# Kernel tuning notes

Hardware: AMD Instinct MI355X
Metric: run time of the kernel (lower is better)

Reference implementation:

```python
import jax, jax.numpy as jnp
import numpy as np

B, N, K, NS = 2, 1024, 64, 32          # batch, points, keypoints (top-k), ball-query neighbors
RADIUS = 1.0                            # ball-query radius (sample_and_group)
R_VOX, S_VOX = 2.0, 0.4                 # voxelize search radius / step
NV = int(round(2 * R_VOX / S_VOX)) + 1  # 11 offsets per axis
C = NV ** 3                             # 1331 candidates per keypoint
F = 32                                  # deep feature channels (num_feat)


def _gather(data, idx):
    # data: (B, N, ...) ; idx: (B, ...) int -> (B, idx_shape..., ...)
    return jax.vmap(lambda d, i: d[i])(data, idx)


def setup_inputs() -> dict:
    key = jax.random.key(0)
    ks = jax.random.split(key, 16)
    f = lambda k, s: jax.random.normal(k, s, dtype=jnp.float32)
    return {
        "src_pts": f(ks[0], (B, 6, N)),
        "tgt_pts": f(ks[1], (B, 6, N)),
        "R_init": f(ks[2], (1, 3, 3)),
        "t_init": f(ks[3], (3, 1)),
        # feature-extraction shared MLP (6 -> 32 -> 32)
        "W1": f(ks[4], (6, F)) * 0.4, "b1": jnp.zeros((F,), jnp.float32),
        "W2": f(ks[5], (F, F)) * 0.2, "b2": jnp.zeros((F,), jnp.float32),
        # weighting (saliency) MLP (32 -> 16 -> 1)
        "Ww1": f(ks[6], (F, 16)) * 0.3, "bw1": jnp.zeros((16,), jnp.float32),
        "Ww2": f(ks[7], (16, 1)) * 0.3, "bw2": jnp.zeros((1,), jnp.float32),
        # deep-feature-embedding shared MLP (3+32 -> 32 -> 32)
        "Wd1": f(ks[8], (3 + F, F)) * 0.3, "bd1": jnp.zeros((F,), jnp.float32),
        "Wd2": f(ks[9], (F, F)) * 0.2, "bd2": jnp.zeros((F,), jnp.float32),
    }


def reference(src_pts, tgt_pts, R_init, t_init,
              W1, b1, W2, b2, Ww1, bw1, Ww2, bw2, Wd1, bd1, Wd2, bd2):
    def fe(pts):                                   # shared feature extraction (FE1)
        x = jnp.transpose(pts, (0, 2, 1))          # (B,N,6)
        h = jax.nn.relu(x @ W1 + b1)
        return x[..., :3], jax.nn.relu(h @ W2 + b2)  # xyz (B,N,3), feat (B,N,F)

    def dfe(x):                                    # shared DFE mini-PointNet MLP
        h = jax.nn.relu(x @ Wd1 + bd1)
        return jax.nn.relu(h @ Wd2 + bd2)

    src_xyz_all, src_feat = fe(src_pts)
    tgt_xyz_all, tgt_feat = fe(tgt_pts)

    # ---- weighting layer: per-point saliency, top-K keypoints ----
    score = (jax.nn.relu(src_feat @ Ww1 + bw1) @ Ww2 + bw2)[..., 0]  # (B,N)
    _, key_idx = jax.lax.top_k(score, K)                              # (B,K)

    src_pts_T = jnp.transpose(src_pts, (0, 2, 1))                     # (B,N,6)
    keypts = _gather(src_pts_T, key_idx)                              # (B,K,6)
    kxyz = keypts[..., :3]                                            # (B,K,3)

    # ---- sample_and_group: ball query among keypoints (npoint == K) ----
    sqd = jnp.sum((kxyz[:, :, None] - kxyz[:, None]) ** 2, -1)        # (B,K,K)
    gidx = jnp.broadcast_to(jnp.arange(K), (B, K, K))
    gidx = jnp.where(sqd > RADIUS ** 2, K, gidx)
    gidx = jnp.sort(gidx, -1)[:, :, :NS]
    gidx = jnp.where(gidx == K, gidx[:, :, :1], gidx)                 # (B,K,NS)

    grouped = _gather(kxyz, gidx)                                     # (B,K,NS,3)
    rel = grouped - kxyz[:, :, None]                                  # local coords
    orig_idx = _gather(key_idx, gidx)                                 # (B,K,NS) into N
    keyfeats = _gather(src_feat, orig_idx)                            # (B,K,NS,F)
    src_cat = jnp.concatenate([rel, keyfeats], -1)                    # (B,K,NS,3+F)

    # ---- voxelize: candidate grid around R_init-transformed keypoints ----
    Rm = jnp.broadcast_to(R_init, (B, 3, 3))
    kxyz_t = jnp.einsum('bij,bkj->bki', Rm, kxyz)                     # (B,K,3)
    off = jnp.linspace(-R_VOX, R_VOX, NV, dtype=jnp.float32)
    gx, gy, gz = jnp.meshgrid(off, off, off, indexing='ij')
    grid = jnp.stack([gx, gy, gz], -1).reshape(-1, 3)                 # (C,3)
    cand = kxyz_t[:, :, None, :] + grid                               # (B,K,C,3)

    # ---- 1-NN of each candidate in the target cloud (feature lookup) ----
    cn = jnp.sum(cand ** 2, -1)                                       # (B,K,C)
    tn = jnp.sum(tgt_xyz_all ** 2, -1)                                # (B,N)
    cross = jnp.einsum('bkcd,bnd->bkcn', cand, tgt_xyz_all)           # (B,K,C,N)
    d = cn[..., None] + tn[:, None, None, :] - 2.0 * cross
    nn = jnp.argmin(jax.lax.stop_gradient(d), -1)                     # (B,K,C)
    nn_xyz = _gather(tgt_xyz_all, nn)                                 # (B,K,C,3)
    nn_feat = _gather(tgt_feat, nn)                                   # (B,K,C,F)
    tgt_cat = jnp.concatenate([cand - nn_xyz, nn_feat], -1)           # (B,K,C,3+F)

    # ---- DFE embeddings + corresponding-point generation (CPG) ----
    src_emb = jnp.max(dfe(src_cat), axis=2)                           # (B,K,F)  max over neighbors
    tgt_emb = dfe(tgt_cat)                                            # (B,K,C,F)
    sim = jnp.einsum('bkd,bkcd->bkc', src_emb, tgt_emb)               # (B,K,C)
    w = jax.nn.softmax(sim, -1)
    tgt_vcp = jnp.einsum('bkc,bkcd->bkd', w, cand)                    # (B,K,3)

    return kxyz, tgt_vcp
```

## Files before the change

### kernel.cpp

```cpp
#include <hip/hip_runtime.h>
#include <math.h>

#define BB 2
#define NPTS 1024
#define KK 64
#define NSZ 32
#define CC 1331
#define FF 32
#define RAD2 1.0f
#define NCOL 121
#define NRNG 8

__global__ __launch_bounds__(64)
void k_features(const float* __restrict__ src_pts, const float* __restrict__ tgt_pts,
                const float* __restrict__ W1, const float* __restrict__ b1,
                const float* __restrict__ W2, const float* __restrict__ b2,
                const float* __restrict__ Ww1, const float* __restrict__ bw1,
                const float* __restrict__ Ww2, const float* __restrict__ bw2,
                const float* __restrict__ Wd1, const float* __restrict__ bd1,
                float* __restrict__ src_feat, float* __restrict__ tgt_A,
                float* __restrict__ tgt_m2, float* __restrict__ score)
{
    int gid = blockIdx.x * blockDim.x + threadIdx.x;
    int isTgt = gid >= BB * NPTS;
    int pn = gid & (BB * NPTS - 1);
    int b = pn >> 10, n = pn & 1023;
    const float* pts = isTgt ? tgt_pts : src_pts;
    float p[6];
#pragma unroll
    for (int i = 0; i < 6; i++) p[i] = pts[(b * 6 + i) * NPTS + n];
    float h[FF];
#pragma unroll
    for (int j = 0; j < FF; j++) {
        float a = b1[j];
#pragma unroll
        for (int i = 0; i < 6; i++) a = fmaf(p[i], W1[i * FF + j], a);
        h[j] = fmaxf(a, 0.0f);
    }
    float ft[FF];
#pragma unroll
    for (int j = 0; j < FF; j++) {
        float a = b2[j];
#pragma unroll
        for (int i = 0; i < FF; i++) a = fmaf(h[i], W2[i * FF + j], a);
        ft[j] = fmaxf(a, 0.0f);
    }
    if (isTgt) {
        float x = p[0], y = p[1], z = p[2];
        float4 v; v.x = x; v.y = y; v.z = z; v.w = x * x + y * y + z * z;
        ((float4*)tgt_m2)[b * NPTS + n] = v;
        float av[FF];
#pragma unroll
        for (int j = 0; j < FF; j++) av[j] = bd1[j];
#pragma unroll
        for (int i = 0; i < FF; i++) {
            float fi = ft[i];
#pragma unroll
            for (int j = 0; j < FF; j++)
                av[j] = fmaf(fi, Wd1[(3 + i) * FF + j], av[j]);
        }
#pragma unroll
        for (int j = 0; j < FF; j++) tgt_A[(b * NPTS + n) * FF + j] = av[j];
    } else {
#pragma unroll
        for (int j = 0; j < FF; j++) src_feat[(b * NPTS + n) * FF + j] = ft[j];
        float acc = bw2[0];
#pragma unroll
        for (int j = 0; j < 16; j++) {
            float a = bw1[j];
#pragma unroll
            for (int i = 0; i < FF; i++) a = fmaf(ft[i], Ww1[i * 16 + j], a);
            acc = fmaf(fmaxf(a, 0.0f), Ww2[j], acc);
        }
        score[b * NPTS + n] = acc;
    }
}

__global__ __launch_bounds__(256)
void k_rank(const float* __restrict__ score, const float* __restrict__ src_pts,
            const float* __restrict__ R,
            int* __restrict__ key_idx, float* __restrict__ kxyz,
            float* __restrict__ kxyz_t, float* __restrict__ out_kxyz)
{
    int blk = blockIdx.x;
    int b = blk >> 4;
    int pbase = (blk & 15) << 6;
    int t = threadIdx.x;
    int sub = t & 3;
    int lp = t >> 2;
    int n = pbase + lp;
    __shared__ float sc[NPTS];
    for (int i = t; i < NPTS; i += 256) sc[i] = score[b * NPTS + i];
    __syncthreads();
    float s = sc[n];
    int rank = 0;
#pragma unroll 8
    for (int jj = 0; jj < 256; jj++) {
        int j = (jj << 2) | sub;
        float sj = sc[j];
        bool before = (sj > s) || (sj == s && j < n);
        rank += before ? 1 : 0;
    }
    rank += __shfl_xor(rank, 1, 64);
    rank += __shfl_xor(rank, 2, 64);
    if (sub == 0 && rank < KK) {
        key_idx[b * KK + rank] = n;
        float x = src_pts[(b * 6 + 0) * NPTS + n];
        float y = src_pts[(b * 6 + 1) * NPTS + n];
        float z = src_pts[(b * 6 + 2) * NPTS + n];
        int o = (b * KK + rank) * 3;
        kxyz[o] = x; kxyz[o + 1] = y; kxyz[o + 2] = z;
        out_kxyz[o] = x; out_kxyz[o + 1] = y; out_kxyz[o + 2] = z;
#pragma unroll
        for (int i = 0; i < 3; i++)
            kxyz_t[o + i] = R[i * 3 + 0] * x + R[i * 3 + 1] * y + R[i * 3 + 2] * z;
    }
}

__global__ __launch_bounds__(64)
void k_group_emb(const float* __restrict__ kxyz, const int* __restrict__ key_idx,
                 const float* __restrict__ src_feat,
                 const float* __restrict__ Wd1, const float* __restrict__ bd1,
                 const float* __restrict__ Wd2, const float* __restrict__ bd2,
                 float* __restrict__ src_emb)
{
    int b = blockIdx.x / KK, kk = blockIdx.x % KK;
    int t = threadIdx.x;
    __shared__ float kx[KK][3];
    __shared__ float emb[NSZ][FF];
    kx[t][0] = kxyz[(b * KK + t) * 3 + 0];
    kx[t][1] = kxyz[(b * KK + t) * 3 + 1];
    kx[t][2] = kxyz[(b * KK + t) * 3 + 2];
    __syncthreads();
    float cx = kx[kk][0], cy = kx[kk][1], cz = kx[kk][2];
    float dx = kx[t][0] - cx, dy = kx[t][1] - cy, dz = kx[t][2] - cz;
    float sq = dx * dx + dy * dy + dz * dz;
    unsigned long long mask = __ballot(sq <= RAD2);
    if (t < NSZ) {
        int cnt = __popcll(mask);
        int want = (t < cnt) ? t : 0;
        unsigned long long mm = mask;
        for (int q = 0; q < want; q++) mm &= (mm - 1);
        int g = __ffsll(mm) - 1;
        float xr = kx[g][0] - cx, yr = kx[g][1] - cy, zr = kx[g][2] - cz;
        int orig = key_idx[b * KK + g];
        const float* fz = &src_feat[(b * NPTS + orig) * FF];
        float fr[FF];
#pragma unroll
        for (int i = 0; i < FF; i++) fr[i] = fz[i];
        float h[FF];
#pragma unroll
        for (int j = 0; j < FF; j++) {
            float a = bd1[j];
            a = fmaf(xr, Wd1[0 * FF + j], a);
            a = fmaf(yr, Wd1[1 * FF + j], a);
            a = fmaf(zr, Wd1[2 * FF + j], a);
#pragma unroll
            for (int i = 0; i < FF; i++) a = fmaf(fr[i], Wd1[(3 + i) * FF + j], a);
            h[j] = fmaxf(a, 0.0f);
        }
#pragma unroll
        for (int j = 0; j < FF; j++) {
            float a = bd2[j];
#pragma unroll
            for (int i = 0; i < FF; i++) a = fmaf(h[i], Wd2[i * FF + j], a);
            emb[t][j] = fmaxf(a, 0.0f);
        }
    }
    __syncthreads();
    if (t < FF) {
        float m = emb[0][t];
#pragma unroll
        for (int s2 = 1; s2 < NSZ; s2++) m = fmaxf(m, emb[s2][t]);
        src_emb[(b * KK + kk) * FF + t] = m;
    }
}

__global__ __launch_bounds__(256)
void k_scan(const float* __restrict__ kxyz_t, const float* __restrict__ tgt_m2,
            float2* __restrict__ part)
{
    int bid = blockIdx.x;
    int bk = bid >> 3, r = bid & 7;
    int b = bk >> 6;
    int t = threadIdx.x;
    int u = t >> 7, lt = t & 127;
    __shared__ float4 P[128];
    __shared__ float2 pbuf[2][NCOL][11];
    if (t < 128) P[t] = ((const float4*)tgt_m2)[(b << 10) + (r << 7) + t];
    float kx = kxyz_t[bk * 3 + 0], ky = kxyz_t[bk * 3 + 1], kz = kxyz_t[bk * 3 + 2];
    float kx2 = -2.0f * kx, ky2 = -2.0f * ky, kz2 = -2.0f * kz;
    int p = lt;
    bool active = p < NCOL;
    int pc = active ? p : 0;
    int ixv = pc / 11, iyv = pc - ixv * 11;
    float gx2 = -2.0f * (-2.0f + ixv * 0.4f);
    float gy2 = -2.0f * (-2.0f + iyv * 0.4f);
    float gz2[11];
#pragma unroll
    for (int iz = 0; iz < 11; iz++) gz2[iz] = -2.0f * (-2.0f + iz * 0.4f);
    float best[11]; int bn[11];
#pragma unroll
    for (int iz = 0; iz < 11; iz++) { best[iz] = 3.0e38f; bn[iz] = 0; }
    __syncthreads();
    if (active) {
        const int pb = u << 6;
#pragma unroll 8
        for (int i = 0; i < 64; i++) {
            float4 v = P[pb + i];
            float a = fmaf(kx2, v.x, fmaf(ky2, v.y, fmaf(kz2, v.z, v.w)));
            float e = fmaf(gx2, v.x, fmaf(gy2, v.y, a));
#pragma unroll
            for (int iz = 0; iz < 11; iz++) {
                float d = fmaf(gz2[iz], v.z, e);
                bool l = d < best[iz];
                best[iz] = l ? d : best[iz];
                bn[iz] = l ? i : bn[iz];
            }
        }
#pragma unroll
        for (int iz = 0; iz < 11; iz++)
            pbuf[u][p][iz] = make_float2(best[iz], __int_as_float(bn[iz] + (u << 6)));
    }
    __syncthreads();
    if (u == 0 && active) {
        int cbase = ((bk << 3) + r) * CC + p * 11;
#pragma unroll
        for (int iz = 0; iz < 11; iz++) {
            float2 r0 = pbuf[0][p][iz], r1 = pbuf[1][p][iz];
            float2 m = (r1.x < r0.x) ? r1 : r0;
            part[cbase + iz] = make_float2(m.x,
                __int_as_float(__float_as_int(m.y) + (r << 7)));
        }
    }
}

__global__ __launch_bounds__(256)
void k_mlp(const float2* __restrict__ part, const float* __restrict__ kxyz_t,
           const float* __restrict__ tgt_m2, const float* __restrict__ tgt_A,
           const float* __restrict__ src_emb,
           const float* __restrict__ Wd1,
           const float* __restrict__ Wd2, const float* __restrict__ bd2,
           float* __restrict__ sim)
{
    const int NCH = 6;
    int bid = blockIdx.x;
    int chunk = bid % NCH;
    int bk = bid / NCH;
    int b = bk >> 6;
    int t = threadIdx.x;
    int c = chunk * 256 + t;
    int cc = min(c, CC - 1);
    float2 rb = part[(bk << 3) * CC + cc];
#pragma unroll
    for (int r = 1; r < NRNG; r++) {
        float2 o = part[((bk << 3) + r) * CC + cc];
        if (o.x < rb.x) rb = o;
    }
    int nb = __float_as_int(rb.y);
    float4 nv = ((const float4*)tgt_m2)[(b << 10) + nb];
    const float4* az = (const float4*)&tgt_A[((b << 10) + nb) * FF];
    float h[FF];
#pragma unroll
    for (int i = 0; i < FF / 4; i++) {
        float4 v = az[i];
        h[i * 4 + 0] = v.x; h[i * 4 + 1] = v.y; h[i * 4 + 2] = v.z; h[i * 4 + 3] = v.w;
    }
    int ixv = cc / 121, rem = cc - ixv * 121, iyv = rem / 11, izv = rem - iyv * 11;
    float cx = kxyz_t[bk * 3 + 0] + (-2.0f + ixv * 0.4f);
    float cy = kxyz_t[bk * 3 + 1] + (-2.0f + iyv * 0.4f);
    float cz = kxyz_t[bk * 3 + 2] + (-2.0f + izv * 0.4f);
    float x0 = cx - nv.x, x1 = cy - nv.y, x2 = cz - nv.z;
#pragma unroll
    for (int j = 0; j < FF; j++) {
        float a = h[j];
        a = fmaf(x0, Wd1[0 * FF + j], a);
        a = fmaf(x1, Wd1[1 * FF + j], a);
        a = fmaf(x2, Wd1[2 * FF + j], a);
        h[j] = fmaxf(a, 0.0f);
    }
    float sv = 0.0f;
#pragma unroll
    for (int j = 0; j < FF; j++) {
        float a = bd2[j];
#pragma unroll
        for (int i = 0; i < FF; i++) a = fmaf(h[i], Wd2[i * FF + j], a);
        sv = fmaf(fmaxf(a, 0.0f), src_emb[bk * FF + j], sv);
    }
    if (c < CC) sim[bk * CC + c] = sv;
}

__global__ __launch_bounds__(256)
void k_softmax(const float* __restrict__ sim, const float* __restrict__ kxyz_t,
               float* __restrict__ out_vcp)
{
    int bk = blockIdx.x;
    int t = threadIdx.x;
    __shared__ float red[256];
    __shared__ float4 red4[256];
    float kx = kxyz_t[bk * 3 + 0], ky = kxyz_t[bk * 3 + 1], kz = kxyz_t[bk * 3 + 2];
    float lm = -3.0e38f;
    for (int c = t; c < CC; c += 256) lm = fmaxf(lm, sim[bk * CC + c]);
    red[t] = lm;
    __syncthreads();
    for (int s2 = 128; s2 > 0; s2 >>= 1) {
        if (t < s2) red[t] = fmaxf(red[t], red[t + s2]);
        __syncthreads();
    }
    float m = red[0];
    float se = 0.f, sx = 0.f, sy = 0.f, sz = 0.f;
    for (int c = t; c < CC; c += 256) {
        float e = expf(sim[bk * CC + c] - m);
        int ix = c / 121, rem = c - ix * 121, iy = rem / 11, iz = rem - iy * 11;
        float cxx = kx + (-2.0f + ix * 0.4f);
        float cyy = ky + (-2.0f + iy * 0.4f);
        float czz = kz + (-2.0f + iz * 0.4f);
        se += e;
        sx = fmaf(e, cxx, sx);
        sy = fmaf(e, cyy, sy);
        sz = fmaf(e, czz, sz);
    }
    red4[t] = make_float4(se, sx, sy, sz);
    __syncthreads();
    for (int s2 = 128; s2 > 0; s2 >>= 1) {
        if (t < s2) {
            float4 a = red4[t], bq = red4[t + s2];
            red4[t] = make_float4(a.x + bq.x, a.y + bq.y, a.z + bq.z, a.w + bq.w);
        }
        __syncthreads();
    }
    if (t == 0) {
        float4 r = red4[0];
        out_vcp[bk * 3 + 0] = r.y / r.x;
        out_vcp[bk * 3 + 1] = r.z / r.x;
        out_vcp[bk * 3 + 2] = r.w / r.x;
    }
}

extern "C" void kernel_launch(void* const* d_in, const int* in_sizes, int n_in,
                              void* d_out, int out_size, void* d_ws, size_t ws_size,
                              hipStream_t stream)
{
    (void)in_sizes; (void)n_in; (void)out_size; (void)ws_size;
    const float* src_pts = (const float*)d_in[0];
    const float* tgt_pts = (const float*)d_in[1];
    const float* R_init  = (const float*)d_in[2];
    const float* W1  = (const float*)d_in[4];
    const float* b1  = (const float*)d_in[5];
    const float* W2  = (const float*)d_in[6];
    const float* b2  = (const float*)d_in[7];
    const float* Ww1 = (const float*)d_in[8];
    const float* bw1 = (const float*)d_in[9];
    const float* Ww2 = (const float*)d_in[10];
    const float* bw2 = (const float*)d_in[11];
    const float* Wd1 = (const float*)d_in[12];
    const float* bd1 = (const float*)d_in[13];
    const float* Wd2 = (const float*)d_in[14];
    const float* bd2 = (const float*)d_in[15];

    float* ws = (float*)d_ws;
    float* src_feat = ws;
    float* tgt_A    = src_feat + BB * NPTS * FF;
    float* tgt_m2   = tgt_A + BB * NPTS * FF;
    float* score    = tgt_m2 + BB * NPTS * 4;
    int*   key_idx  = (int*)(score + BB * NPTS);
    float* kxyz     = (float*)(key_idx + BB * KK);
    float* kxyz_t   = kxyz + BB * KK * 3;
    float* src_emb  = kxyz_t + BB * KK * 3;
    float* sim      = src_emb + BB * KK * FF;
    float2* part    = (float2*)(sim + BB * KK * CC);

    float* out_kxyz = (float*)d_out;
    float* out_vcp  = out_kxyz + BB * KK * 3;

    k_features<<<64, 64, 0, stream>>>(
        src_pts, tgt_pts, W1, b1, W2, b2, Ww1, bw1, Ww2, bw2, Wd1, bd1,
        src_feat, tgt_A, tgt_m2, score);
    k_rank<<<BB * 16, 256, 0, stream>>>(score, src_pts, R_init,
                                        key_idx, kxyz, kxyz_t, out_kxyz);
    k_group_emb<<<BB * KK, 64, 0, stream>>>(kxyz, key_idx, src_feat,
                                            Wd1, bd1, Wd2, bd2, src_emb);
    k_scan<<<BB * KK * NRNG, 256, 0, stream>>>(kxyz_t, tgt_m2, part);
    k_mlp<<<BB * KK * 6, 256, 0, stream>>>(part, kxyz_t, tgt_m2, tgt_A, src_emb,
                                           Wd1, Wd2, bd2, sim);
    k_softmax<<<BB * KK, 256, 0, stream>>>(sim, kxyz_t, out_vcp);
}
```

Measured before the change: 74.97 us.

## Fuse source grouping embedding into MLP kernel and halve scan range splits

Removes the separate k_group_emb launch and recomputes the source-keypoint DFE embedding inside each k_mlp block, spreading the 32x32 MLP over all 256 threads through shared memory. Each of the 6 chunk blocks per keypoint now repeats this small computation. Separately, k_scan now splits the target points into 4 ranges of 256 instead of 8 ranges of 128. That halves the partial results k_mlp has to reduce and the number of scan blocks, at the cost of longer per-thread loops and less parallelism.

Result: faster. 71.20 us (-5.0%).

```diff
diff --git a/kernel.cpp b/kernel.cpp
--- a/kernel.cpp
+++ b/kernel.cpp
@@ -9,7 +9,7 @@
 #define FF 32
 #define RAD2 1.0f
 #define NCOL 121
-#define NRNG 8
+#define NRNG 4
 
 __global__ __launch_bounds__(64)
 void k_features(const float* __restrict__ src_pts, const float* __restrict__ tgt_pts,
@@ -117,82 +117,22 @@
     }
 }
 
-__global__ __launch_bounds__(64)
-void k_group_emb(const float* __restrict__ kxyz, const int* __restrict__ key_idx,
-                 const float* __restrict__ src_feat,
-                 const float* __restrict__ Wd1, const float* __restrict__ bd1,
-                 const float* __restrict__ Wd2, const float* __restrict__ bd2,
-                 float* __restrict__ src_emb)
-{
-    int b = blockIdx.x / KK, kk = blockIdx.x % KK;
-    int t = threadIdx.x;
-    __shared__ float kx[KK][3];
-    __shared__ float emb[NSZ][FF];
-    kx[t][0] = kxyz[(b * KK + t) * 3 + 0];
-    kx[t][1] = kxyz[(b * KK + t) * 3 + 1];
-    kx[t][2] = kxyz[(b * KK + t) * 3 + 2];
-    __syncthreads();
-    float cx = kx[kk][0], cy = kx[kk][1], cz = kx[kk][2];
-    float dx = kx[t][0] - cx, dy = kx[t][1] - cy, dz = kx[t][2] - cz;
-    float sq = dx * dx + dy * dy + dz * dz;
-    unsigned long long mask = __ballot(sq <= RAD2);
-    if (t < NSZ) {
-        int cnt = __popcll(mask);
-        int want = (t < cnt) ? t : 0;
-        unsigned long long mm = mask;
-        for (int q = 0; q < want; q++) mm &= (mm - 1);
-        int g = __ffsll(mm) - 1;
-        float xr = kx[g][0] - cx, yr = kx[g][1] - cy, zr = kx[g][2] - cz;
-        int orig = key_idx[b * KK + g];
-        const float* fz = &src_feat[(b * NPTS + orig) * FF];
-        float fr[FF];
-#pragma unroll
-        for (int i = 0; i < FF; i++) fr[i] = fz[i];
-        float h[FF];
-#pragma unroll
-        for (int j = 0; j < FF; j++) {
-            float a = bd1[j];
-            a = fmaf(xr, Wd1[0 * FF + j], a);
-            a = fmaf(yr, Wd1[1 * FF + j], a);
-            a = fmaf(zr, Wd1[2 * FF + j], a);
-#pragma unroll
-            for (int i = 0; i < FF; i++) a = fmaf(fr[i], Wd1[(3 + i) * FF + j], a);
-            h[j] = fmaxf(a, 0.0f);
-        }
-#pragma unroll
-        for (int j = 0; j < FF; j++) {
-            float a = bd2[j];
-#pragma unroll
-            for (int i = 0; i < FF; i++) a = fmaf(h[i], Wd2[i * FF + j], a);
-            emb[t][j] = fmaxf(a, 0.0f);
-        }
-    }
-    __syncthreads();
-    if (t < FF) {
-        float m = emb[0][t];
-#pragma unroll
-        for (int s2 = 1; s2 < NSZ; s2++) m = fmaxf(m, emb[s2][t]);
-        src_emb[(b * KK + kk) * FF + t] = m;
-    }
-}
-
 __global__ __launch_bounds__(256)
 void k_scan(const float* __restrict__ kxyz_t, const float* __restrict__ tgt_m2,
             float2* __restrict__ part)
 {
     int bid = blockIdx.x;
-    int bk = bid >> 3, r = bid & 7;
+    int bk = bid >> 2, r = bid & 3;
     int b = bk >> 6;
     int t = threadIdx.x;
     int u = t >> 7, lt = t & 127;
-    __shared__ float4 P[128];
+    __shared__ float4 P[256];
     __shared__ float2 pbuf[2][NCOL][11];
-    if (t < 128) P[t] = ((const float4*)tgt_m2)[(b << 10) + (r << 7) + t];
+    P[t] = ((const float4*)tgt_m2)[(b << 10) + (r << 8) + t];
     float kx = kxyz_t[bk * 3 + 0], ky = kxyz_t[bk * 3 + 1], kz = kxyz_t[bk * 3 + 2];
     float kx2 = -2.0f * kx, ky2 = -2.0f * ky, kz2 = -2.0f * kz;
-    int p = lt;
-    bool active = p < NCOL;
-    int pc = active ? p : 0;
+    bool active = lt < NCOL;
+    int pc = active ? lt : 0;
     int ixv = pc / 11, iyv = pc - ixv * 11;
     float gx2 = -2.0f * (-2.0f + ixv * 0.4f);
     float gy2 = -2.0f * (-2.0f + iyv * 0.4f);
@@ -204,9 +144,9 @@
     for (int iz = 0; iz < 11; iz++) { best[iz] = 3.0e38f; bn[iz] = 0; }
     __syncthreads();
     if (active) {
-        const int pb = u << 6;
+        const int pb = u << 7;
 #pragma unroll 8
-        for (int i = 0; i < 64; i++) {
+        for (int i = 0; i < 128; i++) {
             float4 v = P[pb + i];
             float a = fmaf(kx2, v.x, fmaf(ky2, v.y, fmaf(kz2, v.z, v.w)));
             float e = fmaf(gx2, v.x, fmaf(gy2, v.y, a));
@@ -220,26 +160,27 @@
         }
 #pragma unroll
         for (int iz = 0; iz < 11; iz++)
-            pbuf[u][p][iz] = make_float2(best[iz], __int_as_float(bn[iz] + (u << 6)));
+            pbuf[u][lt][iz] = make_float2(best[iz], __int_as_float(bn[iz] + (u << 7)));
     }
     __syncthreads();
     if (u == 0 && active) {
-        int cbase = ((bk << 3) + r) * CC + p * 11;
+        int cbase = ((bk << 2) + r) * CC + lt * 11;
 #pragma unroll
         for (int iz = 0; iz < 11; iz++) {
-            float2 r0 = pbuf[0][p][iz], r1 = pbuf[1][p][iz];
+            float2 r0 = pbuf[0][lt][iz], r1 = pbuf[1][lt][iz];
             float2 m = (r1.x < r0.x) ? r1 : r0;
             part[cbase + iz] = make_float2(m.x,
-                __int_as_float(__float_as_int(m.y) + (r << 7)));
+                __int_as_float(__float_as_int(m.y) + (r << 8)));
         }
     }
 }
 
 __global__ __launch_bounds__(256)
 void k_mlp(const float2* __restrict__ part, const float* __restrict__ kxyz_t,
+           const float* __restrict__ kxyz, const int* __restrict__ key_idx,
+           const float* __restrict__ src_feat,
            const float* __restrict__ tgt_m2, const float* __restrict__ tgt_A,
-           const float* __restrict__ src_emb,
-           const float* __restrict__ Wd1,
+           const float* __restrict__ Wd1, const float* __restrict__ bd1,
            const float* __restrict__ Wd2, const float* __restrict__ bd2,
            float* __restrict__ sim)
 {
@@ -247,14 +188,81 @@
     int bid = blockIdx.x;
     int chunk = bid % NCH;
     int bk = bid / NCH;
-    int b = bk >> 6;
+    int b = bk >> 6, kk = bk & 63;
     int t = threadIdx.x;
+    __shared__ float kxs[KK][3];
+    __shared__ int gidx[NSZ];
+    __shared__ float hb[NSZ][FF + 1];
+    __shared__ float eb[NSZ][FF + 1];
+    __shared__ float semb[FF];
+    if (t < KK) {
+        kxs[t][0] = kxyz[(b * KK + t) * 3 + 0];
+        kxs[t][1] = kxyz[(b * KK + t) * 3 + 1];
+        kxs[t][2] = kxyz[(b * KK + t) * 3 + 2];
+    }
+    __syncthreads();
+    if (t < KK) {
+        float cx = kxs[kk][0], cy = kxs[kk][1], cz = kxs[kk][2];
+        float dx = kxs[t][0] - cx, dy = kxs[t][1] - cy, dz = kxs[t][2] - cz;
+        float sq = dx * dx + dy * dy + dz * dz;
+        unsigned long long mask = __ballot(sq <= RAD2);
+        if (t < NSZ) {
+            int cnt = __popcll(mask);
+            int want = (t < cnt) ? t : 0;
+            unsigned long long mm = mask;
+            for (int q = 0; q < want; q++) mm &= (mm - 1);
+            gidx[t] = __ffsll(mm) - 1;
+        }
+    }
+    __syncthreads();
+    {
+        int s = t >> 3, jb = (t & 7) << 2;
+        int g = gidx[s];
+        float cx = kxs[kk][0], cy = kxs[kk][1], cz = kxs[kk][2];
+        float xr = kxs[g][0] - cx, yr = kxs[g][1] - cy, zr = kxs[g][2] - cz;
+        int orig = key_idx[b * KK + g];
+        const float* fz = &src_feat[(b * NPTS + orig) * FF];
+        float fr[FF];
+#pragma unroll
+        for (int i = 0; i < FF; i++) fr[i] = fz[i];
+#pragma unroll
+        for (int jj = 0; jj < 4; jj++) {
+            int j = jb + jj;
+            float a = bd1[j];
+            a = fmaf(xr, Wd1[0 * FF + j], a);
+            a = fmaf(yr, Wd1[1 * FF + j], a);
+            a = fmaf(zr, Wd1[2 * FF + j], a);
+#pragma unroll
+            for (int i = 0; i < FF; i++) a = fmaf(fr[i], Wd1[(3 + i) * FF + j], a);
+            hb[s][j] = fmaxf(a, 0.0f);
+        }
+    }
+    __syncthreads();
+    {
+        int s = t >> 3, jb = (t & 7) << 2;
+#pragma unroll
+        for (int jj = 0; jj < 4; jj++) {
+            int j = jb + jj;
+            float a = bd2[j];
+#pragma unroll
+            for (int i = 0; i < FF; i++) a = fmaf(hb[s][i], Wd2[i * FF + j], a);
+            eb[s][j] = fmaxf(a, 0.0f);
+        }
+    }
+    __syncthreads();
+    if (t < FF) {
+        float m = eb[0][t];
+#pragma unroll
+        for (int s2 = 1; s2 < NSZ; s2++) m = fmaxf(m, eb[s2][t]);
+        semb[t] = m;
+    }
+    __syncthreads();
     int c = chunk * 256 + t;
     int cc = min(c, CC - 1);
-    float2 rb = part[(bk << 3) * CC + cc];
+    float2 rb = part[(bk << 2) * CC + cc];
 #pragma unroll
     for (int r = 1; r < NRNG; r++) {
-        float2 o = part[((bk << 3) + r) * CC + cc];
+        float2 o = part[((bk << 2) + r) * CC + cc];
         if (o.x < rb.x) rb = o;
     }
     int nb = __float_as_int(rb.y);
@@ -285,7 +293,7 @@
         float a = bd2[j];
 #pragma unroll
         for (int i = 0; i < FF; i++) a = fmaf(h[i], Wd2[i * FF + j], a);
-        sv = fmaf(fmaxf(a, 0.0f), src_emb[bk * FF + j], sv);
+        sv = fmaf(fmaxf(a, 0.0f), semb[j], sv);
     }
     if (c < CC) sim[bk * CC + c] = sv;
 }
@@ -366,8 +374,7 @@
     int*   key_idx  = (int*)(score + BB * NPTS);
     float* kxyz     = (float*)(key_idx + BB * KK);
     float* kxyz_t   = kxyz + BB * KK * 3;
-    float* src_emb  = kxyz_t + BB * KK * 3;
-    float* sim      = src_emb + BB * KK * FF;
+    float* sim      = kxyz_t + BB * KK * 3;
     float2* part    = (float2*)(sim + BB * KK * CC);
 
     float* out_kxyz = (float*)d_out;
@@ -378,10 +385,8 @@
         src_feat, tgt_A, tgt_m2, score);
     k_rank<<<BB * 16, 256, 0, stream>>>(score, src_pts, R_init,
                                         key_idx, kxyz, kxyz_t, out_kxyz);
-    k_group_emb<<<BB * KK, 64, 0, stream>>>(kxyz, key_idx, src_feat,
-                                            Wd1, bd1, Wd2, bd2, src_emb);
     k_scan<<<BB * KK * NRNG, 256, 0, stream>>>(kxyz_t, tgt_m2, part);
-    k_mlp<<<BB * KK * 6, 256, 0, stream>>>(part, kxyz_t, tgt_m2, tgt_A, src_emb,
-                                           Wd1, Wd2, bd2, sim);
+    k_mlp<<<BB * KK * 6, 256, 0, stream>>>(part, kxyz_t, kxyz, key_idx, src_feat,
+                                           tgt_m2, tgt_A, Wd1, bd1, Wd2, bd2, sim);
     k_softmax<<<BB * KK, 256, 0, stream>>>(sim, kxyz_t, out_vcp);
 }
```
